# Performance work log

Hardware: AMD Instinct MI355X
Metric: run time of the kernel (lower is better)

## Reference

```python
import jax, jax.numpy as jnp
import numpy as np

LN_EPS = 1e-5

def _layernorm(x, g, b):
    mu = jnp.mean(x, axis=-1, keepdims=True)
    var = jnp.var(x, axis=-1, keepdims=True)
    return (x - mu) * jax.lax.rsqrt(var + LN_EPS) * g + b

def setup_inputs() -> dict:
    key = jax.random.key(0)
    ks = jax.random.split(key, 8)
    B, N, n, m, a = 4096, 50000, 1024, 16384, 256
    return {
        "x": jax.random.normal(ks[0], (B, n), dtype=jnp.float32),
        "X_data": jax.random.normal(ks[1], (N, n), dtype=jnp.float32),
        "memory_indices": jax.random.randint(ks[2], (m,), 0, N, dtype=jnp.int64)
            if jax.config.jax_enable_x64 else jax.random.randint(ks[2], (m,), 0, N, dtype=jnp.int32),
        "W_q": jax.random.normal(ks[3], (a, n), dtype=jnp.float32) / np.sqrt(n),
        "W_k": jax.random.normal(ks[4], (a, n), dtype=jnp.float32) / np.sqrt(n),
        "W_v": jax.random.normal(ks[5], (n, n), dtype=jnp.float32) / np.sqrt(n),
        "g_q": jnp.ones((a,), jnp.float32), "b_q": jnp.zeros((a,), jnp.float32),
        "g_k": jnp.ones((a,), jnp.float32), "b_k": jnp.zeros((a,), jnp.float32),
        "g_v": jnp.ones((n,), jnp.float32), "b_v": jnp.zeros((n,), jnp.float32),
    }

def reference(x, X_data, memory_indices, W_q, W_k, W_v, g_q, b_q, g_k, b_k, g_v, b_v):
    # Gather memory bank rows: [m, n]
    X_cross = X_data[memory_indices]
    n = x.shape[-1]
    # preprocess(): scalar normalizer so mean row norm ~= sqrt(n) (SAE convention)
    C = jnp.mean(jnp.linalg.norm(X_cross, axis=-1)) / jnp.sqrt(jnp.asarray(n, x.dtype))
    X_cross = X_cross / C
    xs = x / C
    # QKV projections (Linear, no bias) + per-stream LayerNorm
    q = _layernorm(xs @ W_q.T, g_q, b_q)        # [B, a]
    k = _layernorm(X_cross @ W_k.T, g_k, b_k)   # [m, a]
    v = _layernorm(X_cross @ W_v.T, g_v, b_v)   # [m, n]
    # scaled dot-product attention over the memory bank
    scale = 1.0 / np.sqrt(q.shape[-1])
    attn = jax.nn.softmax(jnp.einsum('ba,ma->bm', q, k) * scale, axis=-1)  # [B, m]
    x_hat = attn @ v                             # [B, n]
    return (xs, x_hat, attn, v)
```

## Files before the change

kernel.cpp:

```cpp
#include <hip/hip_runtime.h>
#include <math.h>

typedef _Float16 hlf4 __attribute__((ext_vector_type(4)));
typedef _Float16 hlf8 __attribute__((ext_vector_type(8)));
typedef float f32x4 __attribute__((ext_vector_type(4)));

static __device__ __forceinline__ void gl_lds16(const void* g, void* l) {
    __builtin_amdgcn_global_load_lds(
        (const __attribute__((address_space(1))) unsigned int*)g,
        (__attribute__((address_space(3))) unsigned int*)l, 16, 0, 0);
}

static __device__ __forceinline__ float blk_sum(float v) {
    __shared__ float sm[256];
    int tid = threadIdx.x;
    sm[tid] = v; __syncthreads();
#pragma unroll
    for (int s = 128; s > 0; s >>= 1) {
        if (tid < s) sm[tid] += sm[tid + s];
        __syncthreads();
    }
    float r = sm[0]; __syncthreads();
    return r;
}

static __device__ __forceinline__ float blk_max(float v) {
    __shared__ float sm[256];
    int tid = threadIdx.x;
    sm[tid] = v; __syncthreads();
#pragma unroll
    for (int s = 128; s > 0; s >>= 1) {
        if (tid < s) sm[tid] = fmaxf(sm[tid], sm[tid + s]);
        __syncthreads();
    }
    float r = sm[0]; __syncthreads();
    return r;
}

__global__ __launch_bounds__(256) void k_row_norms(
    const float* __restrict__ X, const int* __restrict__ idx,
    float* __restrict__ norms, int n) {
    long long r = idx[blockIdx.x];
    const float* xr = X + r * (long long)n;
    float s = 0.f;
    for (int k = threadIdx.x * 4; k < n; k += 256 * 4) {
        float4 v = *(const float4*)(xr + k);
        s = fmaf(v.x, v.x, s); s = fmaf(v.y, v.y, s);
        s = fmaf(v.z, v.z, s); s = fmaf(v.w, v.w, s);
    }
    float tot = blk_sum(s);
    if (threadIdx.x == 0) norms[blockIdx.x] = sqrtf(tot);
}

__global__ __launch_bounds__(256) void k_cinv(
    const float* __restrict__ norms, int m, int n, float* __restrict__ cinv) {
    float s = 0.f;
    for (int i = threadIdx.x; i < m; i += 256) s += norms[i];
    float tot = blk_sum(s);
    if (threadIdx.x == 0) cinv[0] = (float)m * sqrtf((float)n) / tot;
}

__global__ __launch_bounds__(256) void k_scale2(
    const float* __restrict__ x, const float* __restrict__ cinv,
    float* __restrict__ y, _Float16* __restrict__ yh, long long total4) {
    float c = cinv[0];
    long long i = blockIdx.x * 256ll + threadIdx.x;
    long long stride = (long long)gridDim.x * 256ll;
    for (; i < total4; i += stride) {
        float4 v = ((const float4*)x)[i];
        v.x *= c; v.y *= c; v.z *= c; v.w *= c;
        ((float4*)y)[i] = v;
        hlf4 o = {(_Float16)v.x, (_Float16)v.y, (_Float16)v.z, (_Float16)v.w};
        ((hlf4*)yh)[i] = o;
    }
}

__global__ __launch_bounds__(256) void k_gather_cvt(
    const float* __restrict__ X, const int* __restrict__ idx,
    const float* __restrict__ cinv, _Float16* __restrict__ out, int n) {
    long long r = idx[blockIdx.x];
    float c = cinv[0];
    const float* src = X + r * (long long)n;
    _Float16* dst = out + (long long)blockIdx.x * n;
    for (int k = threadIdx.x * 4; k < n; k += 256 * 4) {
        float4 v = *(const float4*)(src + k);
        hlf4 o = {(_Float16)(v.x * c), (_Float16)(v.y * c),
                  (_Float16)(v.z * c), (_Float16)(v.w * c)};
        *(hlf4*)(dst + k) = o;
    }
}

__global__ __launch_bounds__(256) void k_cvt(
    const float* __restrict__ in, _Float16* __restrict__ out, long long n4,
    float sc) {
    long long i = blockIdx.x * 256ll + threadIdx.x;
    long long stride = (long long)gridDim.x * 256ll;
    for (; i < n4; i += stride) {
        float4 v = ((const float4*)in)[i];
        hlf4 o = {(_Float16)(v.x * sc), (_Float16)(v.y * sc),
                  (_Float16)(v.z * sc), (_Float16)(v.w * sc)};
        ((hlf4*)out)[i] = o;
    }
}

__global__ __launch_bounds__(256) void k_tcvt(
    const float* __restrict__ in, _Float16* __restrict__ out, int R, int Cc) {
    __shared__ _Float16 t[32][34];
    int tx = threadIdx.x & 31, ty = threadIdx.x >> 5;
    int c0 = blockIdx.x * 32, r0 = blockIdx.y * 32;
#pragma unroll
    for (int i = 0; i < 32; i += 8)
        t[ty + i][tx] = (_Float16)in[(long long)(r0 + ty + i) * Cc + c0 + tx];
    __syncthreads();
#pragma unroll
    for (int i = 0; i < 32; i += 8)
        out[(long long)(c0 + ty + i) * R + r0 + tx] = t[tx][ty + i];
}

__global__ __launch_bounds__(256) void k_gemm4(
    const _Float16* __restrict__ A, int lda,
    const _Float16* __restrict__ B, int ldb,
    float* __restrict__ Cc, long long ldc, int K,
    float* __restrict__ part, long long zstride) {
    __shared__ _Float16 Ah[2][4096];
    __shared__ _Float16 Bh[2][4096];
    const int tid = threadIdx.x;
    const long long m0 = (long long)blockIdx.x * 128;
    const long long n0 = (long long)blockIdx.y * 128;
    const int KC = K / gridDim.z;
    const int kbase = blockIdx.z * KC;
    const int lane = tid & 63, wv = tid >> 6;
    const int wm = (wv >> 1) * 64, wn = (wv & 1) * 64;
    const int fr = lane & 15, fq = lane >> 4;

    const int s0 = tid, s1 = tid + 256;
    const int r0s = s0 >> 2, r1s = s1 >> 2;
    const int g0 = (((s0 & 3) ^ (r0s & 3)) << 3);
    const int g1 = (((s1 & 3) ^ (r1s & 3)) << 3);
    const _Float16* A0 = A + (m0 + r0s) * (long long)lda + kbase + g0;
    const _Float16* A1 = A + (m0 + r1s) * (long long)lda + kbase + g1;
    const _Float16* B0 = B + (n0 + r0s) * (long long)ldb + kbase + g0;
    const _Float16* B1 = B + (n0 + r1s) * (long long)ldb + kbase + g1;

    f32x4 acc[4][4] = {};

    const int NT = KC / 32;
    {
        gl_lds16(A0, &Ah[0][wv * 512]);
        gl_lds16(A1, &Ah[0][2048 + wv * 512]);
        gl_lds16(B0, &Bh[0][wv * 512]);
        gl_lds16(B1, &Bh[0][2048 + wv * 512]);
    }
    __syncthreads();

    for (int kt = 0; kt < NT; ++kt) {
        const int cur = kt & 1;
        if (kt + 1 < NT) {
            const int nx = cur ^ 1;
            const long long ko = (long long)(kt + 1) * 32;
            gl_lds16(A0 + ko, &Ah[nx][wv * 512]);
            gl_lds16(A1 + ko, &Ah[nx][2048 + wv * 512]);
            gl_lds16(B0 + ko, &Bh[nx][wv * 512]);
            gl_lds16(B1 + ko, &Bh[nx][2048 + wv * 512]);
        }
        hlf8 af[4], bf[4];
#pragma unroll
        for (int i = 0; i < 4; ++i) {
            const int r = wm + i * 16 + fr;
            af[i] = *(const hlf8*)&Ah[cur][r * 32 + ((fq ^ (r & 3)) << 3)];
        }
#pragma unroll
        for (int j = 0; j < 4; ++j) {
            const int r = wn + j * 16 + fr;
            bf[j] = *(const hlf8*)&Bh[cur][r * 32 + ((fq ^ (r & 3)) << 3)];
        }
#pragma unroll
        for (int i = 0; i < 4; ++i)
#pragma unroll
            for (int j = 0; j < 4; ++j)
                acc[i][j] = __builtin_amdgcn_mfma_f32_16x16x32_f16(af[i], bf[j], acc[i][j], 0, 0, 0);
        __syncthreads();
    }

    float* outp = (gridDim.z == 1) ? Cc : (part + (long long)blockIdx.z * zstride);
#pragma unroll
    for (int i = 0; i < 4; ++i)
#pragma unroll
        for (int j = 0; j < 4; ++j) {
            float* cp = outp + (m0 + wm + i * 16 + fq * 4) * ldc + (n0 + wn + j * 16 + fr);
#pragma unroll
            for (int r = 0; r < 4; ++r) cp[(long long)r * ldc] = acc[i][j][r];
        }
}

template <int OUT16>
__global__ __launch_bounds__(512, 2) void k_g256(
    const _Float16* __restrict__ A, int lda,
    const _Float16* __restrict__ B, int ldb,
    void* __restrict__ Cc, long long ldc, int K,
    float* __restrict__ part, long long zstride) {
    __shared__ _Float16 Ah[2][16384];
    __shared__ _Float16 Bh[2][16384];
    const int tid = threadIdx.x, lane = tid & 63, wv = tid >> 6;

    const int gx = gridDim.x, gy = gridDim.y;
    int lin = blockIdx.x + gx * (blockIdx.y + gy * blockIdx.z);
    const int cpx = (gx * gy * (int)gridDim.z) >> 3;
    lin = (lin & 7) * cpx + (lin >> 3);
    const int bx = lin % gx; const int rest = lin / gx;
    const int by = rest % gy, bz = rest / gy;

    const long long m0 = (long long)bx * 256;
    const long long n0 = (long long)by * 256;
    const int KC = K / gridDim.z;
    const int kbase = bz * KC;
    const int wm = (wv >> 2) * 128, wn = (wv & 3) * 64;
    const int fr = lane & 15, fq = lane >> 4;

    const _Float16* srcA[4];
    const _Float16* srcB[4];
#pragma unroll
    for (int j = 0; j < 4; ++j) {
        const int s = j * 512 + tid;
        const int r = s >> 3, p = s & 7;
        const int g = (p ^ (r & 7)) << 3;
        srcA[j] = A + (m0 + r) * (long long)lda + kbase + g;
        srcB[j] = B + (n0 + r) * (long long)ldb + kbase + g;
    }

    f32x4 acc[8][4] = {};

#define ISSUE8(bufi, kt)                                                      \
    {                                                                         \
        const long long ko_ = (long long)(kt) * 64;                           \
        _Float16* la_ = &Ah[bufi][0];                                         \
        _Float16* lb_ = &Bh[bufi][0];                                         \
        gl_lds16(srcA[0] + ko_, la_ + (0 * 512 + wv * 64) * 8);               \
        gl_lds16(srcB[0] + ko_, lb_ + (0 * 512 + wv * 64) * 8);               \
        gl_lds16(srcA[1] + ko_, la_ + (1 * 512 + wv * 64) * 8);               \
        gl_lds16(srcB[1] + ko_, lb_ + (1 * 512 + wv * 64) * 8);               \
        gl_lds16(srcA[2] + ko_, la_ + (2 * 512 + wv * 64) * 8);               \
        gl_lds16(srcB[2] + ko_, lb_ + (2 * 512 + wv * 64) * 8);               \
        gl_lds16(srcA[3] + ko_, la_ + (3 * 512 + wv * 64) * 8);               \
        gl_lds16(srcB[3] + ko_, lb_ + (3 * 512 + wv * 64) * 8);               \
    }

    const int NT = KC / 64;
    ISSUE8(0, 0);
    ISSUE8(1, 1);

    for (int kt = 0; kt < NT; ++kt) {
        const int cur = kt & 1;
        if (kt + 1 < NT) asm volatile("s_waitcnt vmcnt(8)" ::: "memory");
        else             asm volatile("s_waitcnt vmcnt(0)" ::: "memory");
        __builtin_amdgcn_s_barrier();

        hlf8 a0[4][2], a1[4][2], b0[2][2], b1[2][2];
#pragma unroll
        for (int i = 0; i < 4; ++i)
#pragma unroll
            for (int ks = 0; ks < 2; ++ks) {
                const int rr = wm + i * 16 + fr;
                a0[i][ks] = *(const hlf8*)&Ah[cur][rr * 64 + (((ks * 4 + fq) ^ (rr & 7)) << 3)];
            }
#pragma unroll
        for (int jj = 0; jj < 2; ++jj)
#pragma unroll
            for (int ks = 0; ks < 2; ++ks) {
                const int cc = wn + jj * 16 + fr;
                b0[jj][ks] = *(const hlf8*)&Bh[cur][cc * 64 + (((ks * 4 + fq) ^ (cc & 7)) << 3)];
            }
        __builtin_amdgcn_s_barrier();
        asm volatile("s_waitcnt lgkmcnt(0)" ::: "memory");
        __builtin_amdgcn_sched_barrier(0);
        __builtin_amdgcn_s_setprio(1);
#pragma unroll
        for (int i = 0; i < 4; ++i)
#pragma unroll
            for (int jj = 0; jj < 2; ++jj)
#pragma unroll
                for (int ks = 0; ks < 2; ++ks)
                    acc[i][jj] = __builtin_amdgcn_mfma_f32_16x16x32_f16(a0[i][ks], b0[jj][ks], acc[i][jj], 0, 0, 0);
        __builtin_amdgcn_s_setprio(0);
        __builtin_amdgcn_s_barrier();

#pragma unroll
        for (int jj = 0; jj < 2; ++jj)
#pragma unroll
            for (int ks = 0; ks < 2; ++ks) {
                const int cc = wn + (jj + 2) * 16 + fr;
                b1[jj][ks] = *(const hlf8*)&Bh[cur][cc * 64 + (((ks * 4 + fq) ^ (cc & 7)) << 3)];
            }
        __builtin_amdgcn_s_barrier();
        asm volatile("s_waitcnt lgkmcnt(0)" ::: "memory");
        __builtin_amdgcn_sched_barrier(0);
        __builtin_amdgcn_s_setprio(1);
#pragma unroll
        for (int i = 0; i < 4; ++i)
#pragma unroll
            for (int jj = 0; jj < 2; ++jj)
#pragma unroll
                for (int ks = 0; ks < 2; ++ks)
                    acc[i][jj + 2] = __builtin_amdgcn_mfma_f32_16x16x32_f16(a0[i][ks], b1[jj][ks], acc[i][jj + 2], 0, 0, 0);
        __builtin_amdgcn_s_setprio(0);
        __builtin_amdgcn_s_barrier();

#pragma unroll
        for (int i = 0; i < 4; ++i)
#pragma unroll
            for (int ks = 0; ks < 2; ++ks) {
                const int rr = wm + (i + 4) * 16 + fr;
                a1[i][ks] = *(const hlf8*)&Ah[cur][rr * 64 + (((ks * 4 + fq) ^ (rr & 7)) << 3)];
            }
        __builtin_amdgcn_s_barrier();
        asm volatile("s_waitcnt lgkmcnt(0)" ::: "memory");
        __builtin_amdgcn_sched_barrier(0);
        __builtin_amdgcn_s_setprio(1);
#pragma unroll
        for (int i = 0; i < 4; ++i)
#pragma unroll
            for (int jj = 0; jj < 2; ++jj)
#pragma unroll
                for (int ks = 0; ks < 2; ++ks)
                    acc[i + 4][jj] = __builtin_amdgcn_mfma_f32_16x16x32_f16(a1[i][ks], b0[jj][ks], acc[i + 4][jj], 0, 0, 0);
        __builtin_amdgcn_s_setprio(0);
        __builtin_amdgcn_s_barrier();

        if (kt + 2 < NT) ISSUE8(cur, kt + 2);
        __builtin_amdgcn_s_setprio(1);
#pragma unroll
        for (int i = 0; i < 4; ++i)
#pragma unroll
            for (int jj = 0; jj < 2; ++jj)
#pragma unroll
                for (int ks = 0; ks < 2; ++ks)
                    acc[i + 4][jj + 2] = __builtin_amdgcn_mfma_f32_16x16x32_f16(a1[i][ks], b1[jj][ks], acc[i + 4][jj + 2], 0, 0, 0);
        __builtin_amdgcn_s_setprio(0);
    }
#undef ISSUE8

    if constexpr (OUT16) {
        _Float16* op = (_Float16*)Cc;
#pragma unroll
        for (int i = 0; i < 8; ++i)
#pragma unroll
            for (int j = 0; j < 4; ++j) {
                _Float16* cp = op + (m0 + wm + i * 16 + fq * 4) * ldc + (n0 + wn + j * 16 + fr);
#pragma unroll
                for (int r = 0; r < 4; ++r) cp[(long long)r * ldc] = (_Float16)acc[i][j][r];
            }
    } else {
        float* outp = (gridDim.z == 1) ? (float*)Cc : (part + (long long)bz * zstride);
#pragma unroll
        for (int i = 0; i < 8; ++i)
#pragma unroll
            for (int j = 0; j < 4; ++j) {
                float* cp = outp + (m0 + wm + i * 16 + fq * 4) * ldc + (n0 + wn + j * 16 + fr);
#pragma unroll
                for (int r = 0; r < 4; ++r) cp[(long long)r * ldc] = acc[i][j][r];
            }
    }
}

__global__ __launch_bounds__(256) void k_redux(
    const float* __restrict__ part, float* __restrict__ out,
    long long n4, long long zs4, int Z) {
    long long i = blockIdx.x * 256ll + threadIdx.x;
    long long stride = (long long)gridDim.x * 256ll;
    for (; i < n4; i += stride) {
        float4 s = ((const float4*)part)[i];
        for (int z = 1; z < Z; ++z) {
            float4 t = ((const float4*)part)[i + z * zs4];
            s.x += t.x; s.y += t.y; s.z += t.z; s.w += t.w;
        }
        ((float4*)out)[i] = s;
    }
}

template <int CNT>
__global__ __launch_bounds__(256) void k_layernorm(
    float* __restrict__ Y, const float* __restrict__ g,
    const float* __restrict__ b, int W) {
    float* yr = Y + (long long)blockIdx.x * W;
    float v[CNT];
    float s = 0.f;
#pragma unroll
    for (int i = 0; i < CNT; ++i) {
        v[i] = yr[threadIdx.x + (i << 8)];
        s += v[i];
    }
    float mu = blk_sum(s) / (float)W;
    float sq = 0.f;
#pragma unroll
    for (int i = 0; i < CNT; ++i) {
        float d = v[i] - mu;
        sq = fmaf(d, d, sq);
    }
    float var = blk_sum(sq) / (float)W;
    float rs = rsqrtf(var + 1e-5f);
#pragma unroll
    for (int i = 0; i < CNT; ++i) {
        int col = threadIdx.x + (i << 8);
        yr[col] = (v[i] - mu) * rs * g[col] + b[col];
    }
}

__global__ __launch_bounds__(256) void k_softmax_h(
    _Float16* __restrict__ Sh, float* __restrict__ attnf) {
    _Float16* sr = Sh + (long long)blockIdx.x * 16384;
    float* ar = attnf + (long long)blockIdx.x * 16384;
    float4 r[16];
    float mx = -1e30f;
#pragma unroll
    for (int i = 0; i < 16; ++i) {
        hlf4 h = ((const hlf4*)sr)[threadIdx.x + (i << 8)];
        float4 t = {(float)h[0], (float)h[1], (float)h[2], (float)h[3]};
        r[i] = t;
        mx = fmaxf(mx, fmaxf(fmaxf(t.x, t.y), fmaxf(t.z, t.w)));
    }
    mx = blk_max(mx);
    float sum = 0.f;
#pragma unroll
    for (int i = 0; i < 16; ++i) {
        float4 t = r[i];
        t.x = __expf(t.x - mx); t.y = __expf(t.y - mx);
        t.z = __expf(t.z - mx); t.w = __expf(t.w - mx);
        r[i] = t;
        sum += t.x + t.y + t.z + t.w;
    }
    sum = blk_sum(sum);
    float inv = 1.0f / sum;
#pragma unroll
    for (int i = 0; i < 16; ++i) {
        float4 t = r[i];
        t.x *= inv; t.y *= inv; t.z *= inv; t.w *= inv;
        ((float4*)ar)[threadIdx.x + (i << 8)] = t;
        hlf4 o = {(_Float16)t.x, (_Float16)t.y, (_Float16)t.z, (_Float16)t.w};
        ((hlf4*)sr)[threadIdx.x + (i << 8)] = o;
    }
}

__global__ __launch_bounds__(256) void k_softmax(
    float* __restrict__ S, _Float16* __restrict__ Sh, float scale) {
    float* sr = S + (long long)blockIdx.x * 16384;
    _Float16* shr = Sh ? Sh + (long long)blockIdx.x * 16384 : nullptr;
    float4 r[16];
    float mx = -1e30f;
#pragma unroll
    for (int i = 0; i < 16; ++i) {
        float4 t = ((const float4*)sr)[threadIdx.x + (i << 8)];
        t.x *= scale; t.y *= scale; t.z *= scale; t.w *= scale;
        r[i] = t;
        mx = fmaxf(mx, fmaxf(fmaxf(t.x, t.y), fmaxf(t.z, t.w)));
    }
    mx = blk_max(mx);
    float sum = 0.f;
#pragma unroll
    for (int i = 0; i < 16; ++i) {
        float4 t = r[i];
        t.x = __expf(t.x - mx); t.y = __expf(t.y - mx);
        t.z = __expf(t.z - mx); t.w = __expf(t.w - mx);
        r[i] = t;
        sum += t.x + t.y + t.z + t.w;
    }
    sum = blk_sum(sum);
    float inv = 1.0f / sum;
#pragma unroll
    for (int i = 0; i < 16; ++i) {
        float4 t = r[i];
        t.x *= inv; t.y *= inv; t.z *= inv; t.w *= inv;
        ((float4*)sr)[threadIdx.x + (i << 8)] = t;
        if (shr) {
            hlf4 o = {(_Float16)t.x, (_Float16)t.y, (_Float16)t.z, (_Float16)t.w};
            ((hlf4*)shr)[threadIdx.x + (i << 8)] = o;
        }
    }
}

extern "C" void kernel_launch(void* const* d_in, const int* in_sizes, int n_in,
                              void* d_out, int out_size, void* d_ws, size_t ws_size,
                              hipStream_t stream) {
    const float* x      = (const float*)d_in[0];
    const float* X_data = (const float*)d_in[1];
    const int*   midx   = (const int*)d_in[2];
    const float* W_q    = (const float*)d_in[3];
    const float* W_k    = (const float*)d_in[4];
    const float* W_v    = (const float*)d_in[5];
    const float* g_q    = (const float*)d_in[6];
    const float* b_q    = (const float*)d_in[7];
    const float* g_k    = (const float*)d_in[8];
    const float* b_k    = (const float*)d_in[9];
    const float* g_v    = (const float*)d_in[10];
    const float* b_v    = (const float*)d_in[11];

    const int n  = in_sizes[10];
    const int a  = in_sizes[6];
    const int m  = in_sizes[2];
    const int Bn = in_sizes[0] / n;

    float* out  = (float*)d_out;
    float* xs   = out;
    float* xhat = xs + (long long)Bn * n;
    float* attn = xhat + (long long)Bn * n;
    float* vout = attn + (long long)Bn * m;

    char* wp = (char*)d_ws;
    auto carve = [&](size_t bytes) -> char* {
        char* r = wp; wp += (bytes + 255) & ~(size_t)255; return r;
    };
    float*     norms = (float*)carve((size_t)m * 4);
    float*     cinv  = (float*)carve(16);
    char*      alias0 = wp;
    float*     qmat  = (float*)carve((size_t)Bn * a * 4);
    float*     kmat  = (float*)carve((size_t)m * a * 4);
    _Float16*  xs_h  = (_Float16*)carve((size_t)Bn * n * 2);
    _Float16*  Xc_h  = (_Float16*)carve((size_t)m * n * 2);
    _Float16*  Wq_h  = (_Float16*)carve((size_t)a * n * 2);
    _Float16*  Wk_h  = (_Float16*)carve((size_t)a * n * 2);
    _Float16*  Wv_h  = (_Float16*)carve((size_t)n * n * 2);
    _Float16*  q_h   = (_Float16*)carve((size_t)Bn * a * 2);
    _Float16*  k_h   = (_Float16*)carve((size_t)m * a * 2);
    float*     splitk = (float*)alias0;
    const int  SK = 4;
    _Float16*  vT_h  = (_Float16*)carve((size_t)n * m * 2);
    size_t used = (size_t)(wp - (char*)d_ws);
    _Float16* attn_h = nullptr;
    if (ws_size >= used + (size_t)Bn * m * 2 + 256)
        attn_h = (_Float16*)carve((size_t)Bn * m * 2);

    hipLaunchKernelGGL(k_row_norms, dim3(m), dim3(256), 0, stream, X_data, midx, norms, n);
    hipLaunchKernelGGL(k_cinv, dim3(1), dim3(256), 0, stream, norms, m, n, cinv);

    hipLaunchKernelGGL(k_scale2, dim3(2048), dim3(256), 0, stream,
                       x, cinv, xs, xs_h, (long long)Bn * n / 4);
    hipLaunchKernelGGL(k_gather_cvt, dim3(m), dim3(256), 0, stream,
                       X_data, midx, cinv, Xc_h, n);

    hipLaunchKernelGGL(k_cvt, dim3(256), dim3(256), 0, stream, W_q, Wq_h, (long long)a * n / 4, 1.f);
    hipLaunchKernelGGL(k_cvt, dim3(256), dim3(256), 0, stream, W_k, Wk_h, (long long)a * n / 4, 1.f);
    hipLaunchKernelGGL(k_cvt, dim3(1024), dim3(256), 0, stream, W_v, Wv_h, (long long)n * n / 4, 1.f);

    hipLaunchKernelGGL(k_gemm4, dim3(Bn / 128, a / 128), dim3(256), 0, stream,
                       xs_h, n, Wq_h, n, qmat, a, n, (float*)nullptr, 0ll);
    hipLaunchKernelGGL(k_gemm4, dim3(m / 128, a / 128), dim3(256), 0, stream,
                       Xc_h, n, Wk_h, n, kmat, a, n, (float*)nullptr, 0ll);
    hipLaunchKernelGGL((k_g256<0>), dim3(m / 256, n / 256), dim3(512), 0, stream,
                       Xc_h, n, Wv_h, n, vout, n, n, (float*)nullptr, 0ll);

    float sc = 1.0f / sqrtf((float)a);
    hipLaunchKernelGGL(k_layernorm<1>, dim3(Bn), dim3(256), 0, stream, qmat, g_q, b_q, a);
    hipLaunchKernelGGL(k_layernorm<1>, dim3(m),  dim3(256), 0, stream, kmat, g_k, b_k, a);
    hipLaunchKernelGGL(k_layernorm<4>, dim3(m),  dim3(256), 0, stream, vout, g_v, b_v, n);
    hipLaunchKernelGGL(k_cvt, dim3(1024), dim3(256), 0, stream, qmat, q_h, (long long)Bn * a / 4, sc);
    hipLaunchKernelGGL(k_cvt, dim3(4096), dim3(256), 0, stream, kmat, k_h, (long long)m * a / 4, 1.f);
    hipLaunchKernelGGL(k_tcvt, dim3(n / 32, m / 32), dim3(256), 0, stream, vout, vT_h, m, n);

    long long zstride = (long long)Bn * n;
    if (attn_h) {
        hipLaunchKernelGGL((k_g256<1>), dim3(Bn / 256, m / 256), dim3(512), 0, stream,
                           q_h, a, k_h, a, attn_h, m, a, (float*)nullptr, 0ll);
        hipLaunchKernelGGL(k_softmax_h, dim3(Bn), dim3(256), 0, stream, attn_h, attn);
        hipLaunchKernelGGL((k_g256<0>), dim3(Bn / 256, n / 256, SK), dim3(512), 0, stream,
                           attn_h, m, vT_h, m, xhat, n, m, splitk, zstride);
        hipLaunchKernelGGL(k_redux, dim3(2048), dim3(256), 0, stream,
                           splitk, xhat, (long long)Bn * n / 4, zstride / 4, SK);
    } else {
        hipLaunchKernelGGL((k_g256<0>), dim3(Bn / 256, m / 256), dim3(512), 0, stream,
                           q_h, a, k_h, a, attn, m, a, (float*)nullptr, 0ll);
        hipLaunchKernelGGL(k_softmax, dim3(Bn), dim3(256), 0, stream, attn, (  _Float16*)nullptr, 1.0f);
        _Float16* chunk_h = (_Float16*)splitk;
        for (int cb = 0; cb < 4; ++cb) {
            const float* src = attn + (long long)cb * 1024 * m;
            hipLaunchKernelGGL(k_cvt, dim3(4096), dim3(256), 0, stream,
                               src, chunk_h, (long long)1024 * m / 4, 1.f);
            hipLaunchKernelGGL((k_g256<0>), dim3(1024 / 256, n / 256), dim3(512), 0, stream,
                               chunk_h, m, vT_h, m, xhat + (long long)cb * 1024 * n, n, m,
                               (float*)nullptr, 0ll);
        }
    }
}
```

Baseline: 614.4 us.

## Restructure 256x256 GEMM into a 4-stage K=32 pipeline and drop pre-LayerNorm scaling

The main fp16 MFMA GEMM moves from a double-buffered K=64 loop, which used several barrier-separated sub-phases, to a four-stage ring of K=32 LDS buffers. Each iteration issues the load three tiles ahead, then does one barrier, one fragment load and a full 8x4 MFMA block. The aim is to hide global-to-LDS latency and cut the number of barriers per K step. The launch-bounds occupancy hint of 2 is also removed, which may change register allocation and occupancy. Separately, the fp16 copies of x and the gathered memory rows are no longer multiplied by 1/C. This relies on the following LayerNorm being scale-invariant apart from eps, and lets the gather run before the norm reduction.

```diff
diff --git a/kernel.cpp b/kernel.cpp
--- a/kernel.cpp
+++ b/kernel.cpp
@@ -68,8 +68,8 @@
     long long stride = (long long)gridDim.x * 256ll;
     for (; i < total4; i += stride) {
         float4 v = ((const float4*)x)[i];
-        v.x *= c; v.y *= c; v.z *= c; v.w *= c;
-        ((float4*)y)[i] = v;
+        float4 w = {v.x * c, v.y * c, v.z * c, v.w * c};
+        ((float4*)y)[i] = w;
         hlf4 o = {(_Float16)v.x, (_Float16)v.y, (_Float16)v.z, (_Float16)v.w};
         ((hlf4*)yh)[i] = o;
     }
@@ -77,15 +77,13 @@
 
 __global__ __launch_bounds__(256) void k_gather_cvt(
     const float* __restrict__ X, const int* __restrict__ idx,
-    const float* __restrict__ cinv, _Float16* __restrict__ out, int n) {
+    _Float16* __restrict__ out, int n) {
     long long r = idx[blockIdx.x];
-    float c = cinv[0];
     const float* src = X + r * (long long)n;
     _Float16* dst = out + (long long)blockIdx.x * n;
     for (int k = threadIdx.x * 4; k < n; k += 256 * 4) {
         float4 v = *(const float4*)(src + k);
-        hlf4 o = {(_Float16)(v.x * c), (_Float16)(v.y * c),
-                  (_Float16)(v.z * c), (_Float16)(v.w * c)};
+        hlf4 o = {(_Float16)v.x, (_Float16)v.y, (_Float16)v.z, (_Float16)v.w};
         *(hlf4*)(dst + k) = o;
     }
 }
@@ -194,13 +192,13 @@
 }
 
 template <int OUT16>
-__global__ __launch_bounds__(512, 2) void k_g256(
+__global__ __launch_bounds__(512) void k_g256(
     const _Float16* __restrict__ A, int lda,
     const _Float16* __restrict__ B, int ldb,
     void* __restrict__ Cc, long long ldc, int K,
     float* __restrict__ part, long long zstride) {
-    __shared__ _Float16 Ah[2][16384];
-    __shared__ _Float16 Bh[2][16384];
+    __shared__ _Float16 Ah[4][8192];
+    __shared__ _Float16 Bh[4][8192];
     const int tid = threadIdx.x, lane = tid & 63, wv = tid >> 6;
 
     const int gx = gridDim.x, gy = gridDim.y;
@@ -217,127 +215,66 @@
     const int wm = (wv >> 2) * 128, wn = (wv & 3) * 64;
     const int fr = lane & 15, fq = lane >> 4;
 
-    const _Float16* srcA[4];
-    const _Float16* srcB[4];
-#pragma unroll
-    for (int j = 0; j < 4; ++j) {
-        const int s = j * 512 + tid;
-        const int r = s >> 3, p = s & 7;
-        const int g = (p ^ (r & 7)) << 3;
-        srcA[j] = A + (m0 + r) * (long long)lda + kbase + g;
-        srcB[j] = B + (n0 + r) * (long long)ldb + kbase + g;
-    }
+    const int sI0 = tid, sI1 = tid + 512;
+    const int L0 = sI0 >> 3, p0 = (sI0 & 7) ^ (L0 & 7);
+    const int L1 = sI1 >> 3, p1 = (sI1 & 7) ^ (L1 & 7);
+    const int row0 = L0 + ((p0 >> 2) << 7), kg0 = (p0 & 3) << 3;
+    const int row1 = L1 + ((p1 >> 2) << 7), kg1 = (p1 & 3) << 3;
+    const _Float16* sA0 = A + (m0 + row0) * (long long)lda + kbase + kg0;
+    const _Float16* sA1 = A + (m0 + row1) * (long long)lda + kbase + kg1;
+    const _Float16* sB0 = B + (n0 + row0) * (long long)ldb + kbase + kg0;
+    const _Float16* sB1 = B + (n0 + row1) * (long long)ldb + kbase + kg1;
+    const int dst0 = (wv * 64) * 8;
+    const int dst1 = (512 + wv * 64) * 8;
 
     f32x4 acc[8][4] = {};
-
-#define ISSUE8(bufi, kt)                                                      \
-    {                                                                         \
-        const long long ko_ = (long long)(kt) * 64;                           \
-        _Float16* la_ = &Ah[bufi][0];                                         \
-        _Float16* lb_ = &Bh[bufi][0];                                         \
-        gl_lds16(srcA[0] + ko_, la_ + (0 * 512 + wv * 64) * 8);               \
-        gl_lds16(srcB[0] + ko_, lb_ + (0 * 512 + wv * 64) * 8);               \
-        gl_lds16(srcA[1] + ko_, la_ + (1 * 512 + wv * 64) * 8);               \
-        gl_lds16(srcB[1] + ko_, lb_ + (1 * 512 + wv * 64) * 8);               \
-        gl_lds16(srcA[2] + ko_, la_ + (2 * 512 + wv * 64) * 8);               \
-        gl_lds16(srcB[2] + ko_, lb_ + (2 * 512 + wv * 64) * 8);               \
-        gl_lds16(srcA[3] + ko_, la_ + (3 * 512 + wv * 64) * 8);               \
-        gl_lds16(srcB[3] + ko_, lb_ + (3 * 512 + wv * 64) * 8);               \
-    }
-
-    const int NT = KC / 64;
-    ISSUE8(0, 0);
-    ISSUE8(1, 1);
-
+    const int NT = KC / 32;
+
+#define STAGE(kt3)                                                        \
+    if ((kt3) < NT) {                                                     \
+        const int bb_ = (kt3) & 3;                                        \
+        const long long ko_ = (long long)(kt3) * 32;                      \
+        gl_lds16(sA0 + ko_, &Ah[bb_][dst0]);                              \
+        gl_lds16(sB0 + ko_, &Bh[bb_][dst0]);                              \
+        gl_lds16(sA1 + ko_, &Ah[bb_][dst1]);                              \
+        gl_lds16(sB1 + ko_, &Bh[bb_][dst1]);                              \
+    }
+
+    STAGE(0); STAGE(1); STAGE(2);
+
+    const int abit = (wm >> 7) << 2;
     for (int kt = 0; kt < NT; ++kt) {
-        const int cur = kt & 1;
-        if (kt + 1 < NT) asm volatile("s_waitcnt vmcnt(8)" ::: "memory");
-        else             asm volatile("s_waitcnt vmcnt(0)" ::: "memory");
+        if (kt + 2 < NT)      asm volatile("s_waitcnt vmcnt(8)" ::: "memory");
+        else if (kt + 1 < NT) asm volatile("s_waitcnt vmcnt(4)" ::: "memory");
+        else                  asm volatile("s_waitcnt vmcnt(0)" ::: "memory");
         __builtin_amdgcn_s_barrier();
-
-        hlf8 a0[4][2], a1[4][2], b0[2][2], b1[2][2];
-#pragma unroll
-        for (int i = 0; i < 4; ++i)
-#pragma unroll
-            for (int ks = 0; ks < 2; ++ks) {
-                const int rr = wm + i * 16 + fr;
-                a0[i][ks] = *(const hlf8*)&Ah[cur][rr * 64 + (((ks * 4 + fq) ^ (rr & 7)) << 3)];
-            }
-#pragma unroll
-        for (int jj = 0; jj < 2; ++jj)
-#pragma unroll
-            for (int ks = 0; ks < 2; ++ks) {
-                const int cc = wn + jj * 16 + fr;
-                b0[jj][ks] = *(const hlf8*)&Bh[cur][cc * 64 + (((ks * 4 + fq) ^ (cc & 7)) << 3)];
-            }
-        __builtin_amdgcn_s_barrier();
-        asm volatile("s_waitcnt lgkmcnt(0)" ::: "memory");
-        __builtin_amdgcn_sched_barrier(0);
+        STAGE(kt + 3);
+
+        const int bb = kt & 3;
+        hlf8 a[8], b[4];
+#pragma unroll
+        for (int i = 0; i < 8; ++i) {
+            const int rr = wm + i * 16 + fr;
+            const int L = rr & 127;
+            const int ph = (abit | fq) ^ (L & 7);
+            a[i] = *(const hlf8*)&Ah[bb][L * 64 + ph * 8];
+        }
+#pragma unroll
+        for (int j = 0; j < 4; ++j) {
+            const int cc = wn + j * 16 + fr;
+            const int L = cc & 127;
+            const int ph = ((((cc >> 7) << 2)) | fq) ^ (L & 7);
+            b[j] = *(const hlf8*)&Bh[bb][L * 64 + ph * 8];
+        }
         __builtin_amdgcn_s_setprio(1);
 #pragma unroll
-        for (int i = 0; i < 4; ++i)
-#pragma unroll
-            for (int jj = 0; jj < 2; ++jj)
-#pragma unroll
-                for (int ks = 0; ks < 2; ++ks)
-                    acc[i][jj] = __builtin_amdgcn_mfma_f32_16x16x32_f16(a0[i][ks], b0[jj][ks], acc[i][jj], 0, 0, 0);
+        for (int i = 0; i < 8; ++i)
+#pragma unroll
+            for (int j = 0; j < 4; ++j)
+                acc[i][j] = __builtin_amdgcn_mfma_f32_16x16x32_f16(a[i], b[j], acc[i][j], 0, 0, 0);
         __builtin_amdgcn_s_setprio(0);
-        __builtin_amdgcn_s_barrier();
-
-#pragma unroll
-        for (int jj = 0; jj < 2; ++jj)
-#pragma unroll
-            for (int ks = 0; ks < 2; ++ks) {
-                const int cc = wn + (jj + 2) * 16 + fr;
-                b1[jj][ks] = *(const hlf8*)&Bh[cur][cc * 64 + (((ks * 4 + fq) ^ (cc & 7)) << 3)];
-            }
-        __builtin_amdgcn_s_barrier();
-        asm volatile("s_waitcnt lgkmcnt(0)" ::: "memory");
-        __builtin_amdgcn_sched_barrier(0);
-        __builtin_amdgcn_s_setprio(1);
-#pragma unroll
-        for (int i = 0; i < 4; ++i)
-#pragma unroll
-            for (int jj = 0; jj < 2; ++jj)
-#pragma unroll
-                for (int ks = 0; ks < 2; ++ks)
-                    acc[i][jj + 2] = __builtin_amdgcn_mfma_f32_16x16x32_f16(a0[i][ks], b1[jj][ks], acc[i][jj + 2], 0, 0, 0);
-        __builtin_amdgcn_s_setprio(0);
-        __builtin_amdgcn_s_barrier();
-
-#pragma unroll
-        for (int i = 0; i < 4; ++i)
-#pragma unroll
-            for (int ks = 0; ks < 2; ++ks) {
-                const int rr = wm + (i + 4) * 16 + fr;
-                a1[i][ks] = *(const hlf8*)&Ah[cur][rr * 64 + (((ks * 4 + fq) ^ (rr & 7)) << 3)];
-            }
-        __builtin_amdgcn_s_barrier();
-        asm volatile("s_waitcnt lgkmcnt(0)" ::: "memory");
-        __builtin_amdgcn_sched_barrier(0);
-        __builtin_amdgcn_s_setprio(1);
-#pragma unroll
-        for (int i = 0; i < 4; ++i)
-#pragma unroll
-            for (int jj = 0; jj < 2; ++jj)
-#pragma unroll
-                for (int ks = 0; ks < 2; ++ks)
-                    acc[i + 4][jj] = __builtin_amdgcn_mfma_f32_16x16x32_f16(a1[i][ks], b0[jj][ks], acc[i + 4][jj], 0, 0, 0);
-        __builtin_amdgcn_s_setprio(0);
-        __builtin_amdgcn_s_barrier();
-
-        if (kt + 2 < NT) ISSUE8(cur, kt + 2);
-        __builtin_amdgcn_s_setprio(1);
-#pragma unroll
-        for (int i = 0; i < 4; ++i)
-#pragma unroll
-            for (int jj = 0; jj < 2; ++jj)
-#pragma unroll
-                for (int ks = 0; ks < 2; ++ks)
-                    acc[i + 4][jj + 2] = __builtin_amdgcn_mfma_f32_16x16x32_f16(a1[i][ks], b1[jj][ks], acc[i + 4][jj + 2], 0, 0, 0);
-        __builtin_amdgcn_s_setprio(0);
-    }
-#undef ISSUE8
+    }
+#undef STAGE
 
     if constexpr (OUT16) {
         _Float16* op = (_Float16*)Cc;
@@ -528,13 +465,13 @@
     if (ws_size >= used + (size_t)Bn * m * 2 + 256)
         attn_h = (_Float16*)carve((size_t)Bn * m * 2);
 
+    hipLaunchKernelGGL(k_gather_cvt, dim3(m), dim3(256), 0, stream,
+                       X_data, midx, Xc_h, n);
     hipLaunchKernelGGL(k_row_norms, dim3(m), dim3(256), 0, stream, X_data, midx, norms, n);
     hipLaunchKernelGGL(k_cinv, dim3(1), dim3(256), 0, stream, norms, m, n, cinv);
 
     hipLaunchKernelGGL(k_scale2, dim3(2048), dim3(256), 0, stream,
                        x, cinv, xs, xs_h, (long long)Bn * n / 4);
-    hipLaunchKernelGGL(k_gather_cvt, dim3(m), dim3(256), 0, stream,
-                       X_data, midx, cinv, Xc_h, n);
 
     hipLaunchKernelGGL(k_cvt, dim3(256), dim3(256), 0, stream, W_q, Wq_h, (long long)a * n / 4, 1.f);
     hipLaunchKernelGGL(k_cvt, dim3(256), dim3(256), 0, stream, W_k, Wk_h, (long long)a * n / 4, 1.f);
@@ -567,7 +504,7 @@
     } else {
         hipLaunchKernelGGL((k_g256<0>), dim3(Bn / 256, m / 256), dim3(512), 0, stream,
                            q_h, a, k_h, a, attn, m, a, (float*)nullptr, 0ll);
-        hipLaunchKernelGGL(k_softmax, dim3(Bn), dim3(256), 0, stream, attn, (  _Float16*)nullptr, 1.0f);
+        hipLaunchKernelGGL(k_softmax, dim3(Bn), dim3(256), 0, stream, attn, (_Float16*)nullptr, 1.0f);
         _Float16* chunk_h = (_Float16*)splitk;
         for (int cb = 0; cb < 4; ++cb) {
             const float* src = attn + (long long)cb * 1024 * m;
```

Result: slower. 677.2 us (+10.2%).
